# Performance work log

Measured on AMD Instinct MI355X. Metric: run time of the kernel, lower is better.

The kernel has to match this reference:

```python
import jax, jax.numpy as jnp
import numpy as np
import math

B, S, D, H = 16, 1024, 1024, 16
HD = D // H  # head_dim = 64

def setup_inputs() -> dict:
    key = jax.random.key(0)
    ks = jax.random.split(key, 10)
    def lin_w(k, out_d, in_d):
        bound = 1.0 / math.sqrt(in_d)
        return jax.random.uniform(k, (out_d, in_d), jnp.float32, -bound, bound)
    return {
        "x": jax.random.normal(ks[0], (B, S, D), jnp.float32),
        "attention_mask_indices": jnp.ones((B, S, 1), dtype=bool),
        "wq_w": lin_w(ks[1], D, D), "wq_b": jnp.zeros((D,), jnp.float32),
        "wk_w": lin_w(ks[2], D, D), "wk_b": jnp.zeros((D,), jnp.float32),
        "wv_w": lin_w(ks[3], D, D), "wv_b": jnp.zeros((D,), jnp.float32),
        "wo_w": lin_w(ks[4], D, D), "wo_b": jnp.zeros((D,), jnp.float32),
    }

def reference(x, attention_mask_indices, wq_w, wq_b, wk_w, wk_b, wv_w, wv_b, wo_w, wo_b):
    bsz, seqlen, _ = x.shape
    # torch Linear: y = x @ W^T + b
    xq = (x @ wq_w.T + wq_b).reshape(bsz, seqlen, H, HD)
    xk = (x @ wk_w.T + wk_b).reshape(bsz, seqlen, H, HD)
    xv = (x @ wv_w.T + wv_b).reshape(bsz, seqlen, H, HD)
    # n_kv_heads == n_heads -> repeat_kv is identity
    scores = jnp.einsum("bqhd,bkhd->bhqk", xq, xk) / math.sqrt(HD)
    mask = attention_mask_indices[:, None, None, :, 0]  # [b,1,1,s]
    scores = jnp.where(mask, scores, jnp.finfo(scores.dtype).min)
    probs = jax.nn.softmax(scores.astype(jnp.float32), axis=-1)
    out = jnp.einsum("bhqk,bkhd->bqhd", probs, xv).reshape(bsz, seqlen, D)
    return out @ wo_w.T + wo_b
```

## Files before the change

### kernel.cpp

```cpp
#include <hip/hip_runtime.h>
#include <hip/hip_bf16.h>

typedef __bf16 bf16;
typedef bf16  bf16x4 __attribute__((ext_vector_type(4)));
typedef bf16  bf16x8 __attribute__((ext_vector_type(8)));
typedef float f32x4  __attribute__((ext_vector_type(4)));

#define B_  16
#define S_  1024
#define D_  1024
#define H_  16
#define HD_ 64

typedef __attribute__((address_space(3))) void lds_void_t;
typedef __attribute__((address_space(1))) void g_void_t;
__device__ __forceinline__ void gl_lds16(const void* g, void* l) {
    __builtin_amdgcn_global_load_lds(
        (const g_void_t*)(uintptr_t)g,
        (lds_void_t*)(uint32_t)(uintptr_t)l, 16, 0, 0);
}

#define BARRIER()    asm volatile("s_barrier" ::: "memory")
#define WAIT_LGKM0() do { asm volatile("s_waitcnt lgkmcnt(0)" ::: "memory"); \
                          __builtin_amdgcn_sched_barrier(0); } while (0)
#define WAIT_VM(n)   asm volatile("s_waitcnt vmcnt(" #n ")" ::: "memory")

__global__ __launch_bounds__(256) void cvt_f32_bf16(
    const float* __restrict__ s, bf16* __restrict__ d, int n)
{
    int i = (blockIdx.x * 256 + threadIdx.x) * 8;
    if (i >= n) return;
    f32x4 a = *(const f32x4*)(s + i);
    f32x4 b = *(const f32x4*)(s + i + 4);
    bf16x8 r;
    for (int j = 0; j < 4; j++) { r[j] = (bf16)a[j]; r[4 + j] = (bf16)b[j]; }
    *(bf16x8*)(d + i) = r;
}

template <bool QKV, int NBY, typename TC>
__global__ __launch_bounds__(512) void gemm8(
    const bf16* __restrict__ A, const bf16* __restrict__ Bw,
    const float* __restrict__ b0, const float* __restrict__ b1,
    const float* __restrict__ b2,
    TC* __restrict__ C, int ldc,
    bf16* __restrict__ Qd, bf16* __restrict__ Kd, bf16* __restrict__ Vd)
{
    __shared__ char lds[131072];

    const int tid  = threadIdx.x;
    const int w    = tid >> 6;
    const int lane = tid & 63;
    const int l15  = lane & 15;
    const int quad = lane >> 4;
    const int wm   = w >> 2;
    const int wn   = w & 3;

    const int nwg = gridDim.x;
    const int lin = blockIdx.x;
    const int swz = (lin & 7) * (nwg >> 3) + (lin >> 3);
    const int bx  = swz / NBY;
    const int by  = swz - bx * NBY;
    const int m0  = bx * 256;
    const int n0  = by * 256;

    const int rl0 = w * 16 + (lane >> 3);
    const int rl1 = rl0 + 8;
    const int sc  = (((lane & 7) ^ ((lane >> 3) & 7))) * 16;
    char* const ld0 = (char*)lds + w * 2048;

    const char* aS0; const char* aS1;
    int bidx = 0, m0loc = 0;
    if constexpr (QKV) {
        aS0 = (const char*)A + (size_t)(m0 + rl0) * 2048 + sc;
        aS1 = (const char*)A + (size_t)(m0 + rl1) * 2048 + sc;
    } else {
        bidx  = m0 >> 10; m0loc = m0 & 1023;
        aS0 = (const char*)A + ((size_t)bidx * 16 * 1024 + m0loc + rl0) * 128 + sc;
        aS1 = (const char*)A + ((size_t)bidx * 16 * 1024 + m0loc + rl1) * 128 + sc;
    }
    const char* bS0 = (const char*)Bw + (size_t)(n0 + rl0) * 2048 + sc;
    const char* bS1 = (const char*)Bw + (size_t)(n0 + rl1) * 2048 + sc;

    auto stageA = [&](int slot, int t, int half) {
        size_t go;
        if constexpr (QKV) go = (size_t)half * 262144 + (size_t)t * 128;
        else               go = (size_t)t * 131072 + (size_t)half * 16384;
        gl_lds16(aS0 + go, ld0 + slot * 16384);
        gl_lds16(aS1 + go, ld0 + slot * 16384 + 1024);
    };
    auto stageB = [&](int slot, int t, int half) {
        size_t go = (size_t)half * 262144 + (size_t)t * 128;
        gl_lds16(bS0 + go, ld0 + slot * 16384);
        gl_lds16(bS1 + go, ld0 + slot * 16384 + 1024);
    };

    const int cx0 = ((quad    ) ^ (l15 & 7)) * 16;
    const int cx1 = ((quad | 4) ^ (l15 & 7)) * 16;
    const char* aE0 = (char*)lds + wm * 16384 + l15 * 128 + cx0;
    const char* aE1 = (char*)lds + wm * 16384 + l15 * 128 + cx1;
    const char* bE0 = (char*)lds + 32768 + (wn >> 1) * 16384 + (wn & 1) * 8192
                      + l15 * 128 + cx0;
    const char* bE1 = (char*)lds + 32768 + (wn >> 1) * 16384 + (wn & 1) * 8192
                      + l15 * 128 + cx1;

    bf16x8 aF[8][2], bF[4][2];
    f32x4 acc[8][4];
    #pragma unroll
    for (int i = 0; i < 8; i++)
        #pragma unroll
        for (int j = 0; j < 4; j++)
            acc[i][j] = (f32x4){0.f, 0.f, 0.f, 0.f};

    auto rdA = [&](int mlo, const char* p0, const char* p1) {
        #pragma unroll
        for (int mf = 0; mf < 4; mf++) {
            aF[mlo + mf][0] = *(const bf16x8*)(p0 + (mlo + mf) * 2048);
            aF[mlo + mf][1] = *(const bf16x8*)(p1 + (mlo + mf) * 2048);
        }
    };
    auto rdB = [&](int nlo, const char* p0, const char* p1) {
        #pragma unroll
        for (int nf = 0; nf < 2; nf++) {
            bF[nlo + nf][0] = *(const bf16x8*)(p0 + (nlo + nf) * 2048);
            bF[nlo + nf][1] = *(const bf16x8*)(p1 + (nlo + nf) * 2048);
        }
    };
    auto mfq = [&](int mlo, int nlo) {
        #pragma unroll
        for (int mf = 0; mf < 4; mf++)
            #pragma unroll
            for (int nf = 0; nf < 2; nf++) {
                f32x4 c = acc[mlo + mf][nlo + nf];
                c = __builtin_amdgcn_mfma_f32_16x16x32_bf16(
                        aF[mlo + mf][0], bF[nlo + nf][0], c, 0, 0, 0);
                c = __builtin_amdgcn_mfma_f32_16x16x32_bf16(
                        aF[mlo + mf][1], bF[nlo + nf][1], c, 0, 0, 0);
                acc[mlo + mf][nlo + nf] = c;
            }
    };

#define PH_PRE()  do { BARRIER(); WAIT_LGKM0(); __builtin_amdgcn_s_setprio(1); } while (0)
#define PH_POST() __builtin_amdgcn_s_setprio(0)

    stageA(0, 0, 0); stageA(1, 0, 1); stageB(2, 0, 0); stageB(3, 0, 1);
    stageA(4, 1, 0); stageA(5, 1, 1);
    WAIT_VM(4);
    BARRIER();

    for (int i = 0; i < 7; i++) {
        const int t1 = 2 * i + 1, t2 = 2 * i + 2, t3 = 2 * i + 3;
        rdA(0, aE0, aE1); rdB(0, bE0, bE1);
        stageB(6, t1, 0);
        PH_PRE(); mfq(0, 0); PH_POST(); BARRIER();
        rdA(4, aE0, aE1); rdB(2, bE0, bE1);
        stageB(7, t1, 1);
        PH_PRE(); mfq(0, 2); PH_POST(); BARRIER();
        stageA(0, t2, 0);
        PH_PRE(); mfq(4, 0); PH_POST(); BARRIER();
        stageA(1, t2, 1);
        PH_PRE(); mfq(4, 2); PH_POST(); WAIT_VM(4); BARRIER();
        rdA(0, aE0 + 65536, aE1 + 65536); rdB(0, bE0 + 65536, bE1 + 65536);
        stageB(2, t2, 0);
        PH_PRE(); mfq(0, 0); PH_POST(); BARRIER();
        rdA(4, aE0 + 65536, aE1 + 65536); rdB(2, bE0 + 65536, bE1 + 65536);
        stageB(3, t2, 1);
        PH_PRE(); mfq(0, 2); PH_POST(); BARRIER();
        stageA(4, t3, 0);
        PH_PRE(); mfq(4, 0); PH_POST(); BARRIER();
        stageA(5, t3, 1);
        PH_PRE(); mfq(4, 2); PH_POST(); WAIT_VM(4); BARRIER();
    }

    rdA(0, aE0, aE1); rdB(0, bE0, bE1);
    stageB(6, 15, 0);
    PH_PRE(); mfq(0, 0); PH_POST(); BARRIER();
    rdA(4, aE0, aE1); rdB(2, bE0, bE1);
    stageB(7, 15, 1);
    PH_PRE(); mfq(0, 2); PH_POST(); BARRIER();
    PH_PRE(); mfq(4, 0); PH_POST(); BARRIER();
    PH_PRE(); mfq(4, 2); PH_POST(); WAIT_VM(0); BARRIER();
    rdA(0, aE0 + 65536, aE1 + 65536); rdB(0, bE0 + 65536, bE1 + 65536);
    PH_PRE(); mfq(0, 0); PH_POST(); BARRIER();
    rdA(4, aE0 + 65536, aE1 + 65536); rdB(2, bE0 + 65536, bE1 + 65536);
    PH_PRE(); mfq(0, 2); PH_POST(); BARRIER();
    PH_PRE(); mfq(4, 0); PH_POST(); BARRIER();
    PH_PRE(); mfq(4, 2); PH_POST();

    if constexpr (QKV) {
        const int seg = n0 >> 10;
        const int cb  = n0 & 1023;
        const float* bp = seg == 0 ? b0 : (seg == 1 ? b1 : b2);
        if (seg < 2) {
            bf16* dst = (seg == 0) ? Qd : Kd;
            #pragma unroll
            for (int mf = 0; mf < 8; mf++)
                #pragma unroll
                for (int nf = 0; nf < 4; nf++) {
                    int col = cb + wn * 64 + nf * 16 + l15;
                    int hh = col >> 6, dd = col & 63;
                    float bb = bp[col];
                    #pragma unroll
                    for (int r = 0; r < 4; r++) {
                        int row = m0 + wm * 128 + mf * 16 + quad * 4 + r;
                        int bl = row >> 10, s = row & 1023;
                        dst[((size_t)(bl * 16 + hh) * 1024 + s) * 64 + dd] =
                            (bf16)(acc[mf][nf][r] + bb);
                    }
                }
        } else {
            #pragma unroll
            for (int mf = 0; mf < 8; mf++)
                #pragma unroll
                for (int nf = 0; nf < 4; nf++) {
                    int col = cb + wn * 64 + nf * 16 + l15;
                    int hh = col >> 6, dd = col & 63;
                    float bb = bp[col];
                    int row0 = m0 + wm * 128 + mf * 16 + quad * 4;
                    int bl = row0 >> 10, s0 = row0 & 1023;
                    bf16x4 pk;
                    #pragma unroll
                    for (int r = 0; r < 4; r++) pk[r] = (bf16)(acc[mf][nf][r] + bb);
                    *(bf16x4*)&Vd[(((size_t)(bl * 16 + hh) * 16 + (s0 >> 6)) * 64 + dd) * 64
                                  + (s0 & 63)] = pk;
                }
        }
    } else {
        #pragma unroll
        for (int mf = 0; mf < 8; mf++)
            #pragma unroll
            for (int nf = 0; nf < 4; nf++) {
                int col = n0 + wn * 64 + nf * 16 + l15;
                float bb = b0[col];
                #pragma unroll
                for (int r = 0; r < 4; r++) {
                    int row = m0 + wm * 128 + mf * 16 + quad * 4 + r;
                    C[(size_t)row * ldc + col] = (TC)(acc[mf][nf][r] + bb);
                }
            }
    }
#undef PH_PRE
#undef PH_POST
}

__global__ __launch_bounds__(256) void attn_fused(
    bf16* __restrict__ Qh, const bf16* __restrict__ Kh,
    const bf16* __restrict__ Vt)
{
    const int qt = blockIdx.x, h = blockIdx.y, b = blockIdx.z;
    const int tid  = threadIdx.x;
    const int w    = tid >> 6;
    const int lane = tid & 63;
    const int l15  = lane & 15;
    const int quad = lane >> 4;

    __shared__ bf16 lds[27648];
    bf16* Ks = lds;
    bf16* Vs = lds + 4608;
    bf16* Pw = lds + 9216 + w * 4608;

    const int nIss = (w == 0) ? 3 : 2;
    int gofs[3];
    for (int j = 0; j < nIss; j++) {
        int c = (w + j * 4) * 64 + lane;
        int row = c / 9;
        int o = c - row * 9;
        if (o == 8) o = 0;
        gofs[j] = (row * 8 + o) * 16;
    }

    const float qscale = 0.125f * 1.44269504088896f;
    bf16* Qbase = Qh + ((size_t)(b * 16 + h) * 1024 + qt * 256 + w * 64) * 64;
    bf16x8 aq[4][2];
    for (int mt = 0; mt < 4; mt++)
        for (int c = 0; c < 2; c++) {
            bf16x8 v = *(const bf16x8*)&Qbase[(mt * 16 + l15) * 64 + c * 32 + quad * 8];
            for (int j = 0; j < 8; j++) v[j] = (bf16)((float)v[j] * qscale);
            aq[mt][c] = v;
        }

    bf16x8 ones;
    for (int j = 0; j < 8; j++) ones[j] = (bf16)1.0f;

    f32x4 acc[4][4], accL[4];
    for (int i = 0; i < 4; i++) {
        accL[i] = (f32x4){0.f, 0.f, 0.f, 0.f};
        for (int j = 0; j < 4; j++) acc[i][j] = (f32x4){0.f, 0.f, 0.f, 0.f};
    }

    const bf16* Ktb = Kh + (size_t)(b * 16 + h) * 65536;
    const bf16* Vtb = Vt + (size_t)(b * 16 + h) * 65536;

    for (int kt = 0; kt < 16; kt++) {
        const char* Ktile = (const char*)(Ktb + kt * 4096);
        const char* Vtile = (const char*)(Vtb + kt * 4096);
        for (int j = 0; j < nIss; j++) {
            int issue = w + j * 4;
            gl_lds16(Ktile + gofs[j], (char*)Ks + issue * 1024);
            gl_lds16(Vtile + gofs[j], (char*)Vs + issue * 1024);
        }
        __syncthreads();

        bf16x8 bk[4][2];
        for (int nt = 0; nt < 4; nt++)
            for (int c = 0; c < 2; c++)
                bk[nt][c] = *(const bf16x8*)&Ks[(nt * 16 + l15) * 72 + c * 32 + quad * 8];
        f32x4 sf[4][4];
        for (int mt = 0; mt < 4; mt++)
            for (int nt = 0; nt < 4; nt++) {
                f32x4 z = (f32x4){0.f, 0.f, 0.f, 0.f};
                z = __builtin_amdgcn_mfma_f32_16x16x32_bf16(aq[mt][0], bk[nt][0], z, 0, 0, 0);
                sf[mt][nt] = __builtin_amdgcn_mfma_f32_16x16x32_bf16(aq[mt][1], bk[nt][1], z, 0, 0, 0);
            }

        for (int mt = 0; mt < 4; mt++)
            for (int nt = 0; nt < 4; nt++)
                for (int r = 0; r < 4; r++)
                    Pw[(mt * 16 + quad * 4 + r) * 72 + nt * 16 + l15] =
                        (bf16)__builtin_amdgcn_exp2f(sf[mt][nt][r]);

        asm volatile("s_waitcnt lgkmcnt(0)" ::: "memory");

        bf16x8 pa[4][2];
        for (int mt = 0; mt < 4; mt++)
            for (int c = 0; c < 2; c++)
                pa[mt][c] = *(const bf16x8*)&Pw[(mt * 16 + l15) * 72 + c * 32 + quad * 8];
        for (int mt = 0; mt < 4; mt++) {
            accL[mt] = __builtin_amdgcn_mfma_f32_16x16x32_bf16(pa[mt][0], ones, accL[mt], 0, 0, 0);
            accL[mt] = __builtin_amdgcn_mfma_f32_16x16x32_bf16(pa[mt][1], ones, accL[mt], 0, 0, 0);
        }
        bf16x8 bv[4][2];
        for (int nt = 0; nt < 4; nt++)
            for (int c = 0; c < 2; c++)
                bv[nt][c] = *(const bf16x8*)&Vs[(nt * 16 + l15) * 72 + c * 32 + quad * 8];
        for (int mt = 0; mt < 4; mt++)
            for (int nt = 0; nt < 4; nt++) {
                acc[mt][nt] = __builtin_amdgcn_mfma_f32_16x16x32_bf16(pa[mt][0], bv[nt][0], acc[mt][nt], 0, 0, 0);
                acc[mt][nt] = __builtin_amdgcn_mfma_f32_16x16x32_bf16(pa[mt][1], bv[nt][1], acc[mt][nt], 0, 0, 0);
            }
        __syncthreads();
    }

    for (int mt = 0; mt < 4; mt++)
        for (int r = 0; r < 4; r++) {
            float rl = 1.f / accL[mt][r];
            for (int nt = 0; nt < 4; nt++)
                Qbase[(mt * 16 + quad * 4 + r) * 64 + nt * 16 + l15] =
                    (bf16)(acc[mt][nt][r] * rl);
        }
}

extern "C" void kernel_launch(void* const* d_in, const int* in_sizes, int n_in,
                              void* d_out, int out_size, void* d_ws, size_t ws_size,
                              hipStream_t stream)
{
    const float* x    = (const float*)d_in[0];
    const float* wq_w = (const float*)d_in[2];
    const float* wq_b = (const float*)d_in[3];
    const float* wk_w = (const float*)d_in[4];
    const float* wk_b = (const float*)d_in[5];
    const float* wv_w = (const float*)d_in[6];
    const float* wv_b = (const float*)d_in[7];
    const float* wo_w = (const float*)d_in[8];
    const float* wo_b = (const float*)d_in[9];
    float* out = (float*)d_out;

    const size_t MEL = 1024 * 1024;
    int CH = 16;
    if (ws_size != 0)
        while (CH > 1 && (4 + 4 * (size_t)CH) * MEL * sizeof(bf16) > ws_size) CH >>= 1;

    bf16* wqkvb = (bf16*)d_ws;
    bf16* wob   = wqkvb + 3 * MEL;
    bf16* xb    = wob + MEL;
    bf16* Qh    = xb + (size_t)CH * MEL;
    bf16* Kh    = Qh + (size_t)CH * MEL;
    bf16* Vtb   = Kh + (size_t)CH * MEL;

    dim3 blk(256);
    cvt_f32_bf16<<<512, blk, 0, stream>>>(wq_w, wqkvb,           (int)MEL);
    cvt_f32_bf16<<<512, blk, 0, stream>>>(wk_w, wqkvb + MEL,     (int)MEL);
    cvt_f32_bf16<<<512, blk, 0, stream>>>(wv_w, wqkvb + 2 * MEL, (int)MEL);
    cvt_f32_bf16<<<512, blk, 0, stream>>>(wo_w, wob,             (int)MEL);

    for (int c0 = 0; c0 < B_; c0 += CH) {
        const int Mc = CH * S_;
        cvt_f32_bf16<<<Mc * 1024 / 2048, blk, 0, stream>>>(
            x + (size_t)c0 * S_ * D_, xb, Mc * 1024);

        gemm8<true, 12, bf16><<<dim3((Mc / 256) * 12), dim3(512), 0, stream>>>(
            xb, wqkvb, wq_b, wk_b, wv_b,
            (bf16*)nullptr, 0, Qh, Kh, Vtb);

        attn_fused<<<dim3(4, H_, CH), blk, 0, stream>>>(Qh, Kh, Vtb);

        gemm8<false, 4, float><<<dim3((Mc / 256) * 4), dim3(512), 0, stream>>>(
            Qh, wob, wo_b, nullptr, nullptr,
            out + (size_t)c0 * S_ * D_, 1024, nullptr, nullptr, nullptr);
    }
}
```

Baseline: 424.5 us.

## Software-pipeline LDS fragment reads in GEMM and double-buffer K/V tiles in attention

Result: faster. 396.1 us (-6.7%).

```diff
diff --git a/kernel.cpp b/kernel.cpp
--- a/kernel.cpp
+++ b/kernel.cpp
@@ -20,10 +20,13 @@
         (lds_void_t*)(uint32_t)(uintptr_t)l, 16, 0, 0);
 }
 
-#define BARRIER()    asm volatile("s_barrier" ::: "memory")
-#define WAIT_LGKM0() do { asm volatile("s_waitcnt lgkmcnt(0)" ::: "memory"); \
-                          __builtin_amdgcn_sched_barrier(0); } while (0)
-#define WAIT_VM(n)   asm volatile("s_waitcnt vmcnt(" #n ")" ::: "memory")
+#define BARRIER()     asm volatile("s_barrier" ::: "memory")
+#define WAIT_LGKM(n)  do { asm volatile("s_waitcnt lgkmcnt(" #n ")" ::: "memory"); \
+                           __builtin_amdgcn_sched_barrier(0); } while (0)
+#define WAIT_VM(n)    asm volatile("s_waitcnt vmcnt(" #n ")" ::: "memory")
+#define SCHED_PIN()   __builtin_amdgcn_sched_barrier(0)
+#define PRIO1()       __builtin_amdgcn_s_setprio(1)
+#define PRIO0()       __builtin_amdgcn_s_setprio(0)
 
 __global__ __launch_bounds__(256) void cvt_f32_bf16(
     const float* __restrict__ s, bf16* __restrict__ d, int n)
@@ -38,7 +41,7 @@
 }
 
 template <bool QKV, int NBY, typename TC>
-__global__ __launch_bounds__(512) void gemm8(
+__global__ __launch_bounds__(512, 2) void gemm8(
     const bf16* __restrict__ A, const bf16* __restrict__ Bw,
     const float* __restrict__ b0, const float* __restrict__ b1,
     const float* __restrict__ b2,
@@ -96,14 +99,18 @@
 
     const int cx0 = ((quad    ) ^ (l15 & 7)) * 16;
     const int cx1 = ((quad | 4) ^ (l15 & 7)) * 16;
-    const char* aE0 = (char*)lds + wm * 16384 + l15 * 128 + cx0;
-    const char* aE1 = (char*)lds + wm * 16384 + l15 * 128 + cx1;
-    const char* bE0 = (char*)lds + 32768 + (wn >> 1) * 16384 + (wn & 1) * 8192
-                      + l15 * 128 + cx0;
-    const char* bE1 = (char*)lds + 32768 + (wn >> 1) * 16384 + (wn & 1) * 8192
-                      + l15 * 128 + cx1;
-
-    bf16x8 aF[8][2], bF[4][2];
+    const char* aEv0 = (char*)lds + wm * 16384 + l15 * 128 + cx0;
+    const char* aEv1 = (char*)lds + wm * 16384 + l15 * 128 + cx1;
+    const char* bEv0 = (char*)lds + 32768 + (wn >> 1) * 16384 + (wn & 1) * 8192
+                       + l15 * 128 + cx0;
+    const char* bEv1 = (char*)lds + 32768 + (wn >> 1) * 16384 + (wn & 1) * 8192
+                       + l15 * 128 + cx1;
+    const char* aOd0 = aEv0 + 65536;
+    const char* aOd1 = aEv1 + 65536;
+    const char* bOd0 = bEv0 + 65536;
+    const char* bOd1 = bEv1 + 65536;
+
+    bf16x8 a03[4][2], a47[4][2], bE[4][2], bO[4][2];
     f32x4 acc[8][4];
     #pragma unroll
     for (int i = 0; i < 8; i++)
@@ -111,80 +118,70 @@
         for (int j = 0; j < 4; j++)
             acc[i][j] = (f32x4){0.f, 0.f, 0.f, 0.f};
 
-    auto rdA = [&](int mlo, const char* p0, const char* p1) {
+    auto rdA = [&](bf16x8 (&dst)[4][2], const char* p0, const char* p1, int ro) {
         #pragma unroll
         for (int mf = 0; mf < 4; mf++) {
-            aF[mlo + mf][0] = *(const bf16x8*)(p0 + (mlo + mf) * 2048);
-            aF[mlo + mf][1] = *(const bf16x8*)(p1 + (mlo + mf) * 2048);
-        }
-    };
-    auto rdB = [&](int nlo, const char* p0, const char* p1) {
+            dst[mf][0] = *(const bf16x8*)(p0 + (ro + mf) * 2048);
+            dst[mf][1] = *(const bf16x8*)(p1 + (ro + mf) * 2048);
+        }
+    };
+    auto rdB2 = [&](bf16x8 (&dst)[4][2], int lo, const char* p0, const char* p1) {
         #pragma unroll
         for (int nf = 0; nf < 2; nf++) {
-            bF[nlo + nf][0] = *(const bf16x8*)(p0 + (nlo + nf) * 2048);
-            bF[nlo + nf][1] = *(const bf16x8*)(p1 + (nlo + nf) * 2048);
-        }
-    };
-    auto mfq = [&](int mlo, int nlo) {
+            dst[lo + nf][0] = *(const bf16x8*)(p0 + (lo + nf) * 2048);
+            dst[lo + nf][1] = *(const bf16x8*)(p1 + (lo + nf) * 2048);
+        }
+    };
+    auto mfq = [&](bf16x8 (&af)[4][2], bf16x8 (&bf_)[4][2], int nlo, int mlo) {
         #pragma unroll
         for (int mf = 0; mf < 4; mf++)
             #pragma unroll
             for (int nf = 0; nf < 2; nf++) {
                 f32x4 c = acc[mlo + mf][nlo + nf];
                 c = __builtin_amdgcn_mfma_f32_16x16x32_bf16(
-                        aF[mlo + mf][0], bF[nlo + nf][0], c, 0, 0, 0);
+                        af[mf][0], bf_[nlo + nf][0], c, 0, 0, 0);
                 c = __builtin_amdgcn_mfma_f32_16x16x32_bf16(
-                        aF[mlo + mf][1], bF[nlo + nf][1], c, 0, 0, 0);
+                        af[mf][1], bf_[nlo + nf][1], c, 0, 0, 0);
                 acc[mlo + mf][nlo + nf] = c;
             }
     };
 
-#define PH_PRE()  do { BARRIER(); WAIT_LGKM0(); __builtin_amdgcn_s_setprio(1); } while (0)
-#define PH_POST() __builtin_amdgcn_s_setprio(0)
-
     stageA(0, 0, 0); stageA(1, 0, 1); stageB(2, 0, 0); stageB(3, 0, 1);
+    stageB(6, 1, 0); stageB(7, 1, 1);
     stageA(4, 1, 0); stageA(5, 1, 1);
-    WAIT_VM(4);
+    WAIT_VM(8);
     BARRIER();
-
-    for (int i = 0; i < 7; i++) {
-        const int t1 = 2 * i + 1, t2 = 2 * i + 2, t3 = 2 * i + 3;
-        rdA(0, aE0, aE1); rdB(0, bE0, bE1);
-        stageB(6, t1, 0);
-        PH_PRE(); mfq(0, 0); PH_POST(); BARRIER();
-        rdA(4, aE0, aE1); rdB(2, bE0, bE1);
-        stageB(7, t1, 1);
-        PH_PRE(); mfq(0, 2); PH_POST(); BARRIER();
-        stageA(0, t2, 0);
-        PH_PRE(); mfq(4, 0); PH_POST(); BARRIER();
-        stageA(1, t2, 1);
-        PH_PRE(); mfq(4, 2); PH_POST(); WAIT_VM(4); BARRIER();
-        rdA(0, aE0 + 65536, aE1 + 65536); rdB(0, bE0 + 65536, bE1 + 65536);
-        stageB(2, t2, 0);
-        PH_PRE(); mfq(0, 0); PH_POST(); BARRIER();
-        rdA(4, aE0 + 65536, aE1 + 65536); rdB(2, bE0 + 65536, bE1 + 65536);
-        stageB(3, t2, 1);
-        PH_PRE(); mfq(0, 2); PH_POST(); BARRIER();
-        stageA(4, t3, 0);
-        PH_PRE(); mfq(4, 0); PH_POST(); BARRIER();
-        stageA(5, t3, 1);
-        PH_PRE(); mfq(4, 2); PH_POST(); WAIT_VM(4); BARRIER();
-    }
-
-    rdA(0, aE0, aE1); rdB(0, bE0, bE1);
-    stageB(6, 15, 0);
-    PH_PRE(); mfq(0, 0); PH_POST(); BARRIER();
-    rdA(4, aE0, aE1); rdB(2, bE0, bE1);
-    stageB(7, 15, 1);
-    PH_PRE(); mfq(0, 2); PH_POST(); BARRIER();
-    PH_PRE(); mfq(4, 0); PH_POST(); BARRIER();
-    PH_PRE(); mfq(4, 2); PH_POST(); WAIT_VM(0); BARRIER();
-    rdA(0, aE0 + 65536, aE1 + 65536); rdB(0, bE0 + 65536, bE1 + 65536);
-    PH_PRE(); mfq(0, 0); PH_POST(); BARRIER();
-    rdA(4, aE0 + 65536, aE1 + 65536); rdB(2, bE0 + 65536, bE1 + 65536);
-    PH_PRE(); mfq(0, 2); PH_POST(); BARRIER();
-    PH_PRE(); mfq(4, 0); PH_POST(); BARRIER();
-    PH_PRE(); mfq(4, 2); PH_POST();
+    rdA(a03, aEv0, aEv1, 0);
+
+    for (int i = 0; i < 8; ++i) {
+        const int t2 = (2 * i + 2) & 15, t3 = (2 * i + 3) & 15;
+        rdB2(bE, 0, bEv0, bEv1);
+        WAIT_LGKM(0); PRIO1(); mfq(a03, bE, 0, 0); PRIO0(); BARRIER();
+        rdB2(bE, 2, bEv0, bEv1);
+        SCHED_PIN();
+        rdA(a47, aEv0, aEv1, 4);
+        WAIT_LGKM(8); PRIO1(); mfq(a03, bE, 2, 0); PRIO0();
+        WAIT_VM(0); BARRIER();
+        rdA(a03, aOd0, aOd1, 0);
+        stageB(2, t2, 0); stageB(3, t2, 1);
+        WAIT_LGKM(8); PRIO1(); mfq(a47, bE, 0, 4); PRIO0(); BARRIER();
+        rdB2(bO, 0, bOd0, bOd1);
+        stageA(0, t2, 0); stageA(1, t2, 1);
+        WAIT_LGKM(8); PRIO1(); mfq(a47, bE, 2, 4); PRIO0(); BARRIER();
+        rdB2(bO, 2, bOd0, bOd1);
+        SCHED_PIN();
+        rdA(a47, aOd0, aOd1, 4);
+        WAIT_LGKM(8); PRIO1(); mfq(a03, bO, 0, 0); PRIO0(); BARRIER();
+        stageB(6, t3, 0);
+        WAIT_LGKM(8); PRIO1(); mfq(a03, bO, 2, 0); PRIO0();
+        WAIT_VM(2); BARRIER();
+        rdA(a03, aEv0, aEv1, 0);
+        stageB(7, t3, 1);
+        WAIT_LGKM(8); PRIO1(); mfq(a47, bO, 0, 4); PRIO0(); BARRIER();
+        stageA(4, t3, 0); stageA(5, t3, 1);
+        WAIT_LGKM(8); PRIO1(); mfq(a47, bO, 2, 4); PRIO0();
+        WAIT_VM(4); BARRIER();
+    }
 
     if constexpr (QKV) {
         const int seg = n0 >> 10;
@@ -238,8 +235,6 @@
                 }
             }
     }
-#undef PH_PRE
-#undef PH_POST
 }
 
 __global__ __launch_bounds__(256) void attn_fused(
@@ -253,10 +248,8 @@
     const int l15  = lane & 15;
     const int quad = lane >> 4;
 
-    __shared__ bf16 lds[27648];
-    bf16* Ks = lds;
-    bf16* Vs = lds + 4608;
-    bf16* Pw = lds + 9216 + w * 4608;
+    __shared__ bf16 lds[36864];
+    bf16* Pw = lds + 18432 + w * 4608;
 
     const int nIss = (w == 0) ? 3 : 2;
     int gofs[3];
@@ -290,35 +283,54 @@
     const bf16* Ktb = Kh + (size_t)(b * 16 + h) * 65536;
     const bf16* Vtb = Vt + (size_t)(b * 16 + h) * 65536;
 
-    for (int kt = 0; kt < 16; kt++) {
+    auto stage = [&](int kt, int cur) {
         const char* Ktile = (const char*)(Ktb + kt * 4096);
         const char* Vtile = (const char*)(Vtb + kt * 4096);
+        char* Kd = (char*)lds + cur * 18432;
         for (int j = 0; j < nIss; j++) {
-            int issue = w + j * 4;
-            gl_lds16(Ktile + gofs[j], (char*)Ks + issue * 1024);
-            gl_lds16(Vtile + gofs[j], (char*)Vs + issue * 1024);
-        }
-        __syncthreads();
+            int is = w + j * 4;
+            gl_lds16(Ktile + gofs[j], Kd + is * 1024);
+            gl_lds16(Vtile + gofs[j], Kd + 9216 + is * 1024);
+        }
+    };
+
+    stage(0, 0);
+
+    for (int kt = 0; kt < 16; kt++) {
+        const int cur = kt & 1;
+        if (kt < 15) {
+            stage(kt + 1, cur ^ 1);
+            if (w == 0) { WAIT_VM(6); } else { WAIT_VM(4); }
+        } else {
+            WAIT_VM(0);
+        }
+        BARRIER();
+
+        const bf16* Ks = lds + cur * 9216;
+        const bf16* Vs = Ks + 4608;
 
         bf16x8 bk[4][2];
         for (int nt = 0; nt < 4; nt++)
             for (int c = 0; c < 2; c++)
                 bk[nt][c] = *(const bf16x8*)&Ks[(nt * 16 + l15) * 72 + c * 32 + quad * 8];
+
         f32x4 sf[4][4];
+        for (int nt = 0; nt < 4; nt++)
+            for (int mt = 0; mt < 4; mt++) {
+                f32x4 z = (f32x4){0.f, 0.f, 0.f, 0.f};
+                z = __builtin_amdgcn_mfma_f32_16x16x32_bf16(bk[nt][0], aq[mt][0], z, 0, 0, 0);
+                sf[nt][mt] = __builtin_amdgcn_mfma_f32_16x16x32_bf16(bk[nt][1], aq[mt][1], z, 0, 0, 0);
+            }
+
         for (int mt = 0; mt < 4; mt++)
             for (int nt = 0; nt < 4; nt++) {
-                f32x4 z = (f32x4){0.f, 0.f, 0.f, 0.f};
-                z = __builtin_amdgcn_mfma_f32_16x16x32_bf16(aq[mt][0], bk[nt][0], z, 0, 0, 0);
-                sf[mt][nt] = __builtin_amdgcn_mfma_f32_16x16x32_bf16(aq[mt][1], bk[nt][1], z, 0, 0, 0);
+                bf16x4 pk;
+                for (int r = 0; r < 4; r++)
+                    pk[r] = (bf16)__builtin_amdgcn_exp2f(sf[nt][mt][r]);
+                *(bf16x4*)&Pw[(mt * 16 + l15) * 72 + nt * 16 + quad * 4] = pk;
             }
 
-        for (int mt = 0; mt < 4; mt++)
-            for (int nt = 0; nt < 4; nt++)
-                for (int r = 0; r < 4; r++)
-                    Pw[(mt * 16 + quad * 4 + r) * 72 + nt * 16 + l15] =
-                        (bf16)__builtin_amdgcn_exp2f(sf[mt][nt][r]);
-
-        asm volatile("s_waitcnt lgkmcnt(0)" ::: "memory");
+        WAIT_LGKM(0);
 
         bf16x8 pa[4][2];
         for (int mt = 0; mt < 4; mt++)
@@ -337,7 +349,7 @@
                 acc[mt][nt] = __builtin_amdgcn_mfma_f32_16x16x32_bf16(pa[mt][0], bv[nt][0], acc[mt][nt], 0, 0, 0);
                 acc[mt][nt] = __builtin_amdgcn_mfma_f32_16x16x32_bf16(pa[mt][1], bv[nt][1], acc[mt][nt], 0, 0, 0);
             }
-        __syncthreads();
+        BARRIER();
     }
 
     for (int mt = 0; mt < 4; mt++)
```
